# Kernel tuning notes

Measured on AMD Instinct MI355X. Metric: run time of the kernel, lower is better.

The kernel has to match this reference:

```python
import jax, jax.numpy as jnp
import numpy as np

TOPK = 1024
C = 32
FC0 = 256
EPS_BN = 1e-5
EPS_NORM = 1e-12


def setup_inputs() -> dict:
    key = jax.random.key(0)
    ks = jax.random.split(key, 8)
    B, L = 128, 16384
    N = B * L
    x = jax.random.normal(ks[0], (N, C), dtype=jnp.float32)
    length = jnp.full((B,), L, dtype=jnp.int32)
    # conv1d_1: Conv1d(32, 1, 1) -> weight [1, 32, 1] ~ vector [32], bias [1]
    w_att = jax.random.normal(ks[1], (C,), dtype=jnp.float32) * (1.0 / np.sqrt(C))
    b_att = jnp.zeros((1,), dtype=jnp.float32)
    # bn_1: BatchNorm1d(1) (eval mode: use running stats)
    g1 = jnp.ones((1,), dtype=jnp.float32)
    be1 = jnp.zeros((1,), dtype=jnp.float32)
    rm1 = jnp.zeros((1,), dtype=jnp.float32)
    rv1 = jnp.ones((1,), dtype=jnp.float32)
    # fc_1: Linear(TOPK*C, FC0)
    fan_in = TOPK * C
    W_fc = jax.random.normal(ks[2], (FC0, fan_in), dtype=jnp.float32) * (1.0 / np.sqrt(fan_in))
    b_fc = jnp.zeros((FC0,), dtype=jnp.float32)
    # bn_2: BatchNorm1d(FC0) (eval mode)
    g2 = jnp.ones((FC0,), dtype=jnp.float32)
    be2 = jnp.zeros((FC0,), dtype=jnp.float32)
    rm2 = jnp.zeros((FC0,), dtype=jnp.float32)
    rv2 = jnp.ones((FC0,), dtype=jnp.float32)
    return {"x": x, "length": length, "w_att": w_att, "b_att": b_att,
            "g1": g1, "be1": be1, "rm1": rm1, "rv1": rv1,
            "W_fc": W_fc, "b_fc": b_fc,
            "g2": g2, "be2": be2, "rm2": rm2, "rv2": rv2}


def reference(x, length, w_att, b_att, g1, be1, rm1, rv1, W_fc, b_fc, g2, be2, rm2, rv2):
    B = length.shape[0]
    N = x.shape[0]
    L = N // B  # equal-length segments (sum(length) == N)
    # attention score: 1x1 conv over channels + BatchNorm1d(1) (eval)
    att = x @ w_att + b_att[0]                                   # [N]
    att = (att - rm1[0]) * (g1[0] / jnp.sqrt(rv1[0] + EPS_BN)) + be1[0]
    # per-segment descending sort + take top TOPK == top_k per segment
    att_b = att.reshape(B, L)                                    # [B, L]
    x_b = x.reshape(B, L, C)                                     # [B, L, C]
    _, idx = jax.lax.top_k(att_b, TOPK)                          # [B, TOPK]
    ranked = jnp.take_along_axis(x_b, idx[:, :, None], axis=1)   # [B, TOPK, C]
    flat = ranked.reshape(B, TOPK * C)                           # [B, TOPK*C]
    # fc_1 + bn_2 (eval) + L2 row-normalize
    out = flat @ W_fc.T + b_fc                                   # [B, FC0]
    out = (out - rm2) * (g2 / jnp.sqrt(rv2 + EPS_BN)) + be2
    nrm = jnp.maximum(jnp.linalg.norm(out, axis=1, keepdims=True), EPS_NORM)
    return out / nrm
```

## Files before the change

### kernel.cpp

```cpp
#include <hip/hip_runtime.h>
#include <stdint.h>

#define CC 32
#define TOPK 1024
#define FC0 256

__global__ __launch_bounds__(256)
void k_att(const float* __restrict__ x,
           const float* __restrict__ w_att, const float* __restrict__ b_att,
           uint32_t* __restrict__ key, int N)
{
    __shared__ float tile[256][CC + 1];
    const int t = threadIdx.x;
    const size_t base = (size_t)blockIdx.x * 256;
    const float4* xv = (const float4*)(x + base * CC);
    #pragma unroll
    for (int i = 0; i < 8; ++i) {
        int e = i * 256 + t;
        float4 v = xv[e];
        int r = e >> 3, c4 = (e & 7) * 4;
        tile[r][c4 + 0] = v.x; tile[r][c4 + 1] = v.y;
        tile[r][c4 + 2] = v.z; tile[r][c4 + 3] = v.w;
    }
    __syncthreads();
    float p[8];
    #pragma unroll
    for (int j = 0; j < 8; ++j) {
        float pj = __fmul_rn(tile[t][j], w_att[j]);
        pj = __fmaf_rn(tile[t][8 + j],  w_att[8 + j],  pj);
        pj = __fmaf_rn(tile[t][16 + j], w_att[16 + j], pj);
        pj = __fmaf_rn(tile[t][24 + j], w_att[24 + j], pj);
        p[j] = pj;
    }
    float q0 = __fadd_rn(p[0], p[1]);
    float q1 = __fadd_rn(p[2], p[3]);
    float q2 = __fadd_rn(p[4], p[5]);
    float q3 = __fadd_rn(p[6], p[7]);
    float dot = __fadd_rn(__fadd_rn(q0, q1), __fadd_rn(q2, q3));
    float v = __fadd_rn(dot, b_att[0]);
    uint32_t bits = __float_as_uint(v);
    key[base + t] = (bits & 0x80000000u) ? ~bits : (bits | 0x80000000u);
}

__device__ __forceinline__ uint64_t cex(uint64_t v, int s, bool up, int t)
{
    uint64_t o = (uint64_t)__shfl_xor((unsigned long long)v, s, 64);
    bool left = ((t & s) == 0);
    uint64_t mn = v < o ? v : o;
    uint64_t mx = v < o ? o : v;
    return (left == up) ? mn : mx;
}

__global__ __launch_bounds__(1024)
void k_topk(const uint32_t* __restrict__ key, int* __restrict__ idx_out, int L)
{
    __shared__ uint32_t kv[16384];
    __shared__ uint64_t cv[2048];
    __shared__ uint32_t whist[16][257];
    __shared__ uint32_t hist[257];
    __shared__ uint32_t s_prefix, s_k, s_cnt;
    const int t = threadIdx.x;
    const int b = blockIdx.x;
    const int lane = t & 63;
    const int wid = t >> 6;
    const uint32_t* kseg = key + (size_t)b * L;
    for (int i = t; i < L; i += 1024) kv[i] = kseg[i];
    if (t == 0) { s_prefix = 0; s_k = TOPK; s_cnt = 0; }
    __syncthreads();
    for (int r = 3; r >= 0; --r) {
        for (int i = t; i < 16 * 257; i += 1024) (&whist[0][0])[i] = 0;
        __syncthreads();
        const uint32_t pref = s_prefix;
        const uint32_t k = s_k;
        const int sh = r * 8;
        for (int i = t; i < L; i += 1024) {
            uint32_t u = kv[i];
            if (r == 3 || (u >> (sh + 8)) == pref)
                atomicAdd(&whist[wid][(u >> sh) & 255u], 1u);
        }
        __syncthreads();
        if (t < 256) {
            uint32_t s = 0;
            #pragma unroll
            for (int w = 0; w < 16; ++w) s += whist[w][t];
            hist[t] = s;
        } else if (t == 256) hist[256] = 0;
        __syncthreads();
        #pragma unroll
        for (int off = 1; off < 256; off <<= 1) {
            uint32_t v = 0;
            if (t < 256 && t + off < 256) v = hist[t + off];
            __syncthreads();
            if (t < 256) hist[t] += v;
            __syncthreads();
        }
        if (t < 256) {
            uint32_t st = hist[t], sn = hist[t + 1];
            if (st >= k && sn < k) {
                s_prefix = (pref << 8) | (uint32_t)t;
                s_k = k - sn;
            }
        }
        __syncthreads();
    }
    const uint32_t T = s_prefix;
    for (int i = t; i < L; i += 1024) {
        bool q = kv[i] >= T;
        unsigned long long m = __ballot(q);
        uint32_t base = 0;
        if (lane == 0 && m)
            base = atomicAdd(&s_cnt, (uint32_t)__popcll(m));
        base = __shfl(base, 0);
        if (q) {
            uint32_t pos = base + (uint32_t)__popcll(m & ((1ULL << lane) - 1ULL));
            if (pos < 2048)
                cv[pos] = ((uint64_t)kv[i] << 32) | (uint64_t)(uint32_t)(~(uint32_t)i);
        }
    }
    __syncthreads();
    const uint32_t mm = s_cnt < 2048u ? s_cnt : 2048u;
    for (int i = t; i < 2048; i += 1024)
        if ((uint32_t)i >= mm) cv[i] = 0ULL;
    __syncthreads();
    {
        uint64_t r0 = cv[t], r1 = cv[t + 1024];
        #pragma unroll
        for (int size = 2; size <= 64; size <<= 1) {
            bool up = ((t & size) == 0);
            #pragma unroll
            for (int s = size >> 1; s > 0; s >>= 1) {
                r0 = cex(r0, s, up, t);
                r1 = cex(r1, s, up, t);
            }
        }
        cv[t] = r0; cv[t + 1024] = r1;
    }
    #pragma unroll
    for (int size = 128; size <= 2048; size <<= 1) {
        for (int s = size >> 1; s >= 64; s >>= 1) {
            __syncthreads();
            int i = ((t & ~(s - 1)) << 1) | (t & (s - 1));
            int j = i | s;
            uint64_t va = cv[i], vb = cv[j];
            bool up = ((i & size) == 0);
            if (up ? (va > vb) : (va < vb)) { cv[i] = vb; cv[j] = va; }
        }
        __syncthreads();
        {
            uint64_t a0 = cv[t], a1 = cv[t + 1024];
            bool up0, up1;
            if (size <= 512)      { up0 = ((t & size) == 0); up1 = up0; }
            else if (size == 1024){ up0 = true;  up1 = false; }
            else                  { up0 = true;  up1 = true;  }
            #pragma unroll
            for (int s = 32; s > 0; s >>= 1) {
                a0 = cex(a0, s, up0, t);
                a1 = cex(a1, s, up1, t);
            }
            cv[t] = a0; cv[t + 1024] = a1;
        }
        __syncthreads();
    }
    if (t < TOPK)
        idx_out[(size_t)b * TOPK + t] = (int)(~(uint32_t)cv[2047 - t]);
}

#define FT 128
#define KCI 32
#define NKC 128
#define KCHUNK 256

__global__ __launch_bounds__(256)
void k_fc(const float* __restrict__ x, const int* __restrict__ idx,
          const float* __restrict__ W, float* __restrict__ part, int L)
{
    __shared__ float flT[KCI][128];
    __shared__ float wT[KCI][FT];
    const int t = threadIdx.x;
    const int kc = blockIdx.x;
    const int fb = blockIdx.y * FT;
    const int tb = t >> 4, tf = t & 15;
    float acc[8][8];
    #pragma unroll
    for (int i = 0; i < 8; ++i)
        #pragma unroll
        for (int j = 0; j < 8; ++j) acc[i][j] = 0.f;

    const int b_ld = t >> 1, half = t & 1;
    for (int sub = 0; sub < KCHUNK / KCI; ++sub) {
        const int kbase = kc * KCHUNK + sub * KCI;
        const int t_idx = kbase >> 5;
        {
            int row = idx[b_ld * TOPK + t_idx];
            row = row < 0 ? 0 : (row >= L ? L - 1 : row);
            const float* src = x + ((size_t)b_ld * L + row) * CC + half * 16;
            #pragma unroll
            for (int q = 0; q < 4; ++q) {
                float4 v = ((const float4*)src)[q];
                int c0 = half * 16 + q * 4;
                flT[c0 + 0][b_ld] = v.x; flT[c0 + 1][b_ld] = v.y;
                flT[c0 + 2][b_ld] = v.z; flT[c0 + 3][b_ld] = v.w;
            }
        }
        #pragma unroll
        for (int i2 = 0; i2 < 4; ++i2) {
            int fl = (t >> 3) + i2 * 32;
            int u = t & 7;
            const float4 v = *(const float4*)(W + (size_t)(fb + fl) * (TOPK * CC) + kbase + u * 4);
            wT[u * 4 + 0][fl] = v.x; wT[u * 4 + 1][fl] = v.y;
            wT[u * 4 + 2][fl] = v.z; wT[u * 4 + 3][fl] = v.w;
        }
        __syncthreads();
        #pragma unroll
        for (int kk = 0; kk < KCI; ++kk) {
            float bb[8], ww[8];
            *(float4*)&bb[0] = *(const float4*)&flT[kk][tb * 8];
            *(float4*)&bb[4] = *(const float4*)&flT[kk][tb * 8 + 4];
            *(float4*)&ww[0] = *(const float4*)&wT[kk][tf * 8];
            *(float4*)&ww[4] = *(const float4*)&wT[kk][tf * 8 + 4];
            #pragma unroll
            for (int i = 0; i < 8; ++i)
                #pragma unroll
                for (int j = 0; j < 8; ++j)
                    acc[i][j] = fmaf(bb[i], ww[j], acc[i][j]);
        }
        __syncthreads();
    }
    float* pbase = part + ((size_t)kc * 128) * 256 + fb + tf * 8;
    #pragma unroll
    for (int i = 0; i < 8; ++i) {
        float* dst = pbase + (size_t)(tb * 8 + i) * 256;
        ((float4*)dst)[0] = make_float4(acc[i][0], acc[i][1], acc[i][2], acc[i][3]);
        ((float4*)dst)[1] = make_float4(acc[i][4], acc[i][5], acc[i][6], acc[i][7]);
    }
}

__global__ __launch_bounds__(256)
void k_post(const float* __restrict__ part, const float* __restrict__ b_fc,
            const float* __restrict__ g2, const float* __restrict__ be2,
            const float* __restrict__ rm2, const float* __restrict__ rv2,
            float* __restrict__ out)
{
    __shared__ float red[256];
    const int b = blockIdx.x, f = threadIdx.x;
    float s = 0.f;
    #pragma unroll 8
    for (int kc = 0; kc < NKC; ++kc)
        s += part[((size_t)kc * 128 + b) * 256 + f];
    s += b_fc[f];
    float o = (s - rm2[f]) * (g2[f] / sqrtf(rv2[f] + 1e-5f)) + be2[f];
    red[f] = o * o;
    __syncthreads();
    for (int st = 128; st > 0; st >>= 1) {
        if (f < st) red[f] += red[f + st];
        __syncthreads();
    }
    float nrm = fmaxf(sqrtf(red[0]), 1e-12f);
    out[(size_t)b * 256 + f] = o / nrm;
}

extern "C" void kernel_launch(void* const* d_in, const int* in_sizes, int n_in,
                              void* d_out, int out_size, void* d_ws, size_t ws_size,
                              hipStream_t stream)
{
    const float* x     = (const float*)d_in[0];
    const float* w_att = (const float*)d_in[2];
    const float* b_att = (const float*)d_in[3];
    const float* W_fc  = (const float*)d_in[8];
    const float* b_fc  = (const float*)d_in[9];
    const float* g2    = (const float*)d_in[10];
    const float* be2   = (const float*)d_in[11];
    const float* rm2   = (const float*)d_in[12];
    const float* rv2   = (const float*)d_in[13];

    const int N = in_sizes[0] / CC;
    const int B = in_sizes[1];
    const int L = N / B;

    uint8_t* ws = (uint8_t*)d_ws;
    uint32_t* key = (uint32_t*)(ws);
    int* idx      = (int*)(ws + (size_t)N * 4);
    float* part   = (float*)(ws + (size_t)N * 4 + (size_t)B * TOPK * 4);

    k_att<<<N / 256, 256, 0, stream>>>(x, w_att, b_att, key, N);
    k_topk<<<B, 1024, 0, stream>>>(key, idx, L);
    dim3 g3(NKC, FC0 / FT);
    k_fc<<<g3, 256, 0, stream>>>(x, idx, W_fc, part, L);
    k_post<<<B, 256, 0, stream>>>(part, b_fc, g2, be2, rm2, rv2, (float*)d_out);
}
```

Baseline: 129.8 us.

## Shorten radix top-k select to two rounds and narrow FC feature tile

The top-k radix select now stops after two 8-bit rounds, using a 16-bit prefix threshold that feeds the existing candidate compaction and bitonic sort. It also replaces the per-wave histograms and the barrier-heavy 256-step scan with one shared histogram and a single-wave shuffle scan. Separately, the FC kernel's feature tile shrinks from 128 to 64, so each thread holds 8x4 accumulators and more blocks run. The coarser threshold can admit more than 2048 candidates when the top values share a 16-bit prefix, and those extras are dropped. The smaller FC tile lowers register pressure but gives less reuse of the gathered rows, and the launch grid must match the new tile size.

```diff
diff --git a/kernel.cpp b/kernel.cpp
--- a/kernel.cpp
+++ b/kernel.cpp
@@ -56,44 +56,43 @@
 {
     __shared__ uint32_t kv[16384];
     __shared__ uint64_t cv[2048];
-    __shared__ uint32_t whist[16][257];
     __shared__ uint32_t hist[257];
     __shared__ uint32_t s_prefix, s_k, s_cnt;
     const int t = threadIdx.x;
     const int b = blockIdx.x;
     const int lane = t & 63;
-    const int wid = t >> 6;
     const uint32_t* kseg = key + (size_t)b * L;
     for (int i = t; i < L; i += 1024) kv[i] = kseg[i];
     if (t == 0) { s_prefix = 0; s_k = TOPK; s_cnt = 0; }
     __syncthreads();
-    for (int r = 3; r >= 0; --r) {
-        for (int i = t; i < 16 * 257; i += 1024) (&whist[0][0])[i] = 0;
+    #pragma unroll
+    for (int round = 0; round < 2; ++round) {
+        if (t < 257) hist[t] = 0;
         __syncthreads();
         const uint32_t pref = s_prefix;
         const uint32_t k = s_k;
-        const int sh = r * 8;
         for (int i = t; i < L; i += 1024) {
             uint32_t u = kv[i];
-            if (r == 3 || (u >> (sh + 8)) == pref)
-                atomicAdd(&whist[wid][(u >> sh) & 255u], 1u);
-        }
-        __syncthreads();
-        if (t < 256) {
-            uint32_t s = 0;
-            #pragma unroll
-            for (int w = 0; w < 16; ++w) s += whist[w][t];
-            hist[t] = s;
-        } else if (t == 256) hist[256] = 0;
-        __syncthreads();
-        #pragma unroll
-        for (int off = 1; off < 256; off <<= 1) {
-            uint32_t v = 0;
-            if (t < 256 && t + off < 256) v = hist[t + off];
-            __syncthreads();
-            if (t < 256) hist[t] += v;
-            __syncthreads();
-        }
+            if (round == 0) atomicAdd(&hist[u >> 24], 1u);
+            else if ((u >> 24) == pref) atomicAdd(&hist[(u >> 16) & 255u], 1u);
+        }
+        __syncthreads();
+        if (t < 64) {
+            int l = t;
+            uint32_t h0 = hist[4*l], h1 = hist[4*l+1], h2 = hist[4*l+2], h3 = hist[4*l+3];
+            uint32_t s3 = h3, s2 = h2 + s3, s1 = h1 + s2, s0 = h0 + s1;
+            uint32_t tot = s0, run = tot;
+            #pragma unroll
+            for (int off = 1; off < 64; off <<= 1) {
+                int src = l + off < 64 ? l + off : 63;
+                uint32_t o = __shfl(run, src, 64);
+                if (l + off < 64) run += o;
+            }
+            uint32_t esuf = run - tot;
+            hist[4*l]   = s0 + esuf; hist[4*l+1] = s1 + esuf;
+            hist[4*l+2] = s2 + esuf; hist[4*l+3] = s3 + esuf;
+        }
+        __syncthreads();
         if (t < 256) {
             uint32_t st = hist[t], sn = hist[t + 1];
             if (st >= k && sn < k) {
@@ -103,7 +102,7 @@
         }
         __syncthreads();
     }
-    const uint32_t T = s_prefix;
+    const uint32_t T = s_prefix << 16;
     for (int i = t; i < L; i += 1024) {
         bool q = kv[i] >= T;
         unsigned long long m = __ballot(q);
@@ -165,7 +164,7 @@
         idx_out[(size_t)b * TOPK + t] = (int)(~(uint32_t)cv[2047 - t]);
 }
 
-#define FT 128
+#define FT 64
 #define KCI 32
 #define NKC 128
 #define KCHUNK 256
@@ -180,11 +179,11 @@
     const int kc = blockIdx.x;
     const int fb = blockIdx.y * FT;
     const int tb = t >> 4, tf = t & 15;
-    float acc[8][8];
+    float acc[8][4];
     #pragma unroll
     for (int i = 0; i < 8; ++i)
         #pragma unroll
-        for (int j = 0; j < 8; ++j) acc[i][j] = 0.f;
+        for (int j = 0; j < 4; ++j) acc[i][j] = 0.f;
 
     const int b_ld = t >> 1, half = t & 1;
     for (int sub = 0; sub < KCHUNK / KCI; ++sub) {
@@ -202,36 +201,38 @@
                 flT[c0 + 2][b_ld] = v.z; flT[c0 + 3][b_ld] = v.w;
             }
         }
-        #pragma unroll
-        for (int i2 = 0; i2 < 4; ++i2) {
-            int fl = (t >> 3) + i2 * 32;
-            int u = t & 7;
-            const float4 v = *(const float4*)(W + (size_t)(fb + fl) * (TOPK * CC) + kbase + u * 4);
-            wT[u * 4 + 0][fl] = v.x; wT[u * 4 + 1][fl] = v.y;
-            wT[u * 4 + 2][fl] = v.z; wT[u * 4 + 3][fl] = v.w;
+        {
+            int idx512 = t + 256 * 0;
+            #pragma unroll
+            for (int i2 = 0; i2 < 2; ++i2) {
+                int e = t + i2 * 256;
+                int fl = e >> 3, u = e & 7;
+                const float4 v = *(const float4*)(W + (size_t)(fb + fl) * (TOPK * CC) + kbase + u * 4);
+                wT[u * 4 + 0][fl] = v.x; wT[u * 4 + 1][fl] = v.y;
+                wT[u * 4 + 2][fl] = v.z; wT[u * 4 + 3][fl] = v.w;
+            }
+            (void)idx512;
         }
         __syncthreads();
         #pragma unroll
         for (int kk = 0; kk < KCI; ++kk) {
-            float bb[8], ww[8];
+            float bb[8], ww[4];
             *(float4*)&bb[0] = *(const float4*)&flT[kk][tb * 8];
             *(float4*)&bb[4] = *(const float4*)&flT[kk][tb * 8 + 4];
-            *(float4*)&ww[0] = *(const float4*)&wT[kk][tf * 8];
-            *(float4*)&ww[4] = *(const float4*)&wT[kk][tf * 8 + 4];
+            *(float4*)&ww[0] = *(const float4*)&wT[kk][tf * 4];
             #pragma unroll
             for (int i = 0; i < 8; ++i)
                 #pragma unroll
-                for (int j = 0; j < 8; ++j)
+                for (int j = 0; j < 4; ++j)
                     acc[i][j] = fmaf(bb[i], ww[j], acc[i][j]);
         }
         __syncthreads();
     }
-    float* pbase = part + ((size_t)kc * 128) * 256 + fb + tf * 8;
+    float* pbase = part + ((size_t)kc * 128) * 256 + fb + tf * 4;
     #pragma unroll
     for (int i = 0; i < 8; ++i) {
         float* dst = pbase + (size_t)(tb * 8 + i) * 256;
         ((float4*)dst)[0] = make_float4(acc[i][0], acc[i][1], acc[i][2], acc[i][3]);
-        ((float4*)dst)[1] = make_float4(acc[i][4], acc[i][5], acc[i][6], acc[i][7]);
     }
 }
 
```

After: 116.9 us. -10.0%, faster.
